# Kernel tuning notes

Hardware: AMD Instinct MI355X
Metric: run time of the kernel (lower is better)

Reference implementation:

```python
import jax, jax.numpy as jnp
import numpy as np


def setup_inputs() -> dict:
    key = jax.random.key(0)
    ks = jax.random.split(key, 6)
    B, N, d = 8, 2048, 64
    h = jax.random.normal(ks[0], (B, N, d), dtype=jnp.float32)
    adj = jax.random.randint(ks[1], (B, N, N), 0, 2, dtype=jnp.int32)
    h_root = jax.random.normal(ks[2], (B, N), dtype=jnp.float32)
    weight = jax.random.normal(ks[3], (d, d), dtype=jnp.float32) * (1.0 / np.sqrt(d))
    a1 = jax.random.normal(ks[4], (d, 1), dtype=jnp.float32) * (1.0 / np.sqrt(d))
    a2 = jax.random.normal(ks[5], (d, 1), dtype=jnp.float32) * (1.0 / np.sqrt(d))
    return {"h": h, "adj": adj, "h_root": h_root, "weight": weight, "a1": a1, "a2": a2}


def reference(h, adj, h_root, weight, a1, a2):
    h0 = h
    hw = jax.nn.relu(jnp.matmul(h, weight))          # (B,N,d)
    t1 = jnp.matmul(hw, a1)                          # (B,N,1)
    t2 = jnp.matmul(hw, a2)                          # (B,N,1)
    # e[b,i,j] = relu(t1[b,i] + t2[b,j])  (broadcast, same as repeat/view in torch)
    e = jax.nn.relu(t1 + jnp.swapaxes(t2, -1, -2))   # (B,N,N)
    # FAITHFUL to source bug: pos0 = -9e15 * zeros_like(adj) == 0, so
    # non-edges get logit 0 (not -inf) before softmax.
    e = jnp.where(adj > 0, e, jnp.zeros_like(e))
    attention = jax.nn.softmax(e, axis=-1)           # (B,N,N)
    embedding = jnp.matmul(attention, hw)            # (B,N,d)
    # assign = h_root[:,:,None] @ ones(B,1,d) -> h_root broadcast over d;
    # assign > 0  <=>  h_root > 0 since ones are positive.
    assign = h_root[:, :, None] * jnp.ones((1, 1, hw.shape[-1]), dtype=hw.dtype)
    embedding = jnp.where(assign > 0, embedding, h0)
    return embedding
```

## Files before the change

### kernel.cpp

```cpp
#include <hip/hip_runtime.h>
#include <hip/hip_bf16.h>

#define BATCH 8
#define NN    2048
#define DD    64
#define BN    (BATCH * NN)

#define NSPLIT 8
#define JSPAN  (NN / NSPLIT)
#define KSTEPS (JSPAN / 32)
#define HWST   264

typedef __attribute__((ext_vector_type(8))) short bf16x8;
typedef __attribute__((ext_vector_type(4))) float f32x4;

static __device__ __forceinline__ unsigned f2bf_pk(float lo, float hi) {
  unsigned ul = __float_as_uint(lo);
  unsigned uh = __float_as_uint(hi);
  ul = (ul + 0x7fffu + ((ul >> 16) & 1u)) >> 16;
  uh = (uh + 0x7fffu + ((uh >> 16) & 1u)) & 0xffff0000u;
  return ul | uh;
}

__global__ __launch_bounds__(256) void k1_hw_t1_t2(
    const float* __restrict__ h, const float* __restrict__ W,
    const float* __restrict__ a1, const float* __restrict__ a2,
    unsigned short* __restrict__ hwT, float* __restrict__ t1, float* __restrict__ t2) {
  __shared__ float ht[64 * 36];
  __shared__ float Ws[64 * 64];
  __shared__ unsigned short bt[64 * 40];

  const int t  = threadIdx.x;
  const int r0 = blockIdx.x * 32;

#pragma unroll
  for (int r = 0; r < 4; ++r) {
    int f = t + 256 * r;
    reinterpret_cast<float4*>(Ws)[f] = reinterpret_cast<const float4*>(W)[f];
  }
#pragma unroll
  for (int r = 0; r < 2; ++r) {
    int f = t + 256 * r;
    int i = f >> 4, j4 = f & 15;
    float4 v = reinterpret_cast<const float4*>(h + (size_t)(r0 + i) * DD)[j4];
    ht[(4 * j4 + 0) * 36 + i] = v.x;
    ht[(4 * j4 + 1) * 36 + i] = v.y;
    ht[(4 * j4 + 2) * 36 + i] = v.z;
    ht[(4 * j4 + 3) * 36 + i] = v.w;
  }
  __syncthreads();

  const int trow = t >> 4, kcol = t & 15;
  float4 acc0 = make_float4(0.f, 0.f, 0.f, 0.f);
  float4 acc1 = make_float4(0.f, 0.f, 0.f, 0.f);

#pragma unroll 8
  for (int j = 0; j < 64; ++j) {
    float2 hv = *reinterpret_cast<const float2*>(&ht[j * 36 + 2 * trow]);
    float4 wv = reinterpret_cast<const float4*>(Ws)[j * 16 + kcol];
    acc0.x = fmaf(hv.x, wv.x, acc0.x); acc0.y = fmaf(hv.x, wv.y, acc0.y);
    acc0.z = fmaf(hv.x, wv.z, acc0.z); acc0.w = fmaf(hv.x, wv.w, acc0.w);
    acc1.x = fmaf(hv.y, wv.x, acc1.x); acc1.y = fmaf(hv.y, wv.y, acc1.y);
    acc1.z = fmaf(hv.y, wv.z, acc1.z); acc1.w = fmaf(hv.y, wv.w, acc1.w);
  }

  acc0.x = fmaxf(acc0.x, 0.f); acc0.y = fmaxf(acc0.y, 0.f);
  acc0.z = fmaxf(acc0.z, 0.f); acc0.w = fmaxf(acc0.w, 0.f);
  acc1.x = fmaxf(acc1.x, 0.f); acc1.y = fmaxf(acc1.y, 0.f);
  acc1.z = fmaxf(acc1.z, 0.f); acc1.w = fmaxf(acc1.w, 0.f);

  float4 a1v = reinterpret_cast<const float4*>(a1)[kcol];
  float4 a2v = reinterpret_cast<const float4*>(a2)[kcol];
  float s1_0 = acc0.x * a1v.x + acc0.y * a1v.y + acc0.z * a1v.z + acc0.w * a1v.w;
  float s1_1 = acc1.x * a1v.x + acc1.y * a1v.y + acc1.z * a1v.z + acc1.w * a1v.w;
  float s2_0 = acc0.x * a2v.x + acc0.y * a2v.y + acc0.z * a2v.z + acc0.w * a2v.w;
  float s2_1 = acc1.x * a2v.x + acc1.y * a2v.y + acc1.z * a2v.z + acc1.w * a2v.w;
#pragma unroll
  for (int m = 1; m <= 8; m <<= 1) {
    s1_0 += __shfl_xor(s1_0, m, 64);
    s1_1 += __shfl_xor(s1_1, m, 64);
    s2_0 += __shfl_xor(s2_0, m, 64);
    s2_1 += __shfl_xor(s2_1, m, 64);
  }
  {
    int row = r0 + 2 * trow;
    if (kcol == 0) {
      t1[row] = s1_0; t1[row + 1] = s1_1;
      t2[row] = s2_0; t2[row + 1] = s2_1;
    }
  }

  {
    const float* a0 = &acc0.x;
    const float* a1p = &acc1.x;
#pragma unroll
    for (int c = 0; c < 4; ++c) {
      int k = 4 * kcol + c;
      *reinterpret_cast<unsigned*>(&bt[k * 40 + 2 * trow]) = f2bf_pk(a0[c], a1p[c]);
    }
  }
  __syncthreads();
  {
    int k = t >> 2, jp = t & 3;
    int bb = r0 >> 11;
    int jb = r0 & (NN - 1);
    *reinterpret_cast<int4*>(hwT + ((size_t)bb * DD + k) * NN + jb + jp * 8) =
        *reinterpret_cast<const int4*>(&bt[k * 40 + jp * 8]);
  }
}

__global__ __launch_bounds__(256, 4) void k2_attn(
    const unsigned short* __restrict__ hwT, const int* __restrict__ adj,
    const float* __restrict__ t1, const float* __restrict__ t2,
    float* __restrict__ pacc, float* __restrict__ pden) {
  __shared__ unsigned short hws[64 * HWST];
  __shared__ float t2s[JSPAN];

  const int t     = threadIdx.x;
  const int split = blockIdx.x >> 8;
  const int rem   = blockIdx.x & 255;
  const int b     = rem >> 5;
  const int i0    = (rem & 31) * 64;
  const int w     = t >> 6;
  const int lane  = t & 63;
  const int m     = lane & 15;
  const int quad  = lane >> 4;
  const int jbase = split * JSPAN;

  const unsigned short* hwTb = hwT + (size_t)b * DD * NN + jbase;
#pragma unroll
  for (int r = 0; r < 8; ++r) {
    int idx = t + 256 * r, k = idx >> 5, jp = idx & 31;
    *reinterpret_cast<int4*>(&hws[k * HWST + jp * 8]) =
        *reinterpret_cast<const int4*>(hwTb + (size_t)k * NN + jp * 8);
  }
  if (t < JSPAN / 4)
    *reinterpret_cast<float4*>(&t2s[t * 4]) =
        *reinterpret_cast<const float4*>(t2 + b * NN + jbase + t * 4);

  const float t1v = t1[b * NN + i0 + w * 16 + m];
  const int* adjl = adj + (size_t)(b * NN + i0 + w * 16 + m) * NN + jbase + quad * 8;

  f32x4 acc[4];
#pragma unroll
  for (int g = 0; g < 4; ++g) acc[g] = (f32x4){0.f, 0.f, 0.f, 0.f};
  float den = 0.f;

  int4 a0 = *reinterpret_cast<const int4*>(adjl);
  int4 a1i = *reinterpret_cast<const int4*>(adjl + 4);
  __syncthreads();

#pragma unroll
  for (int ks = 0; ks < KSTEPS; ++ks) {
    int4 n0, n1;
    if (ks + 1 < KSTEPS) {
      const int* ap = adjl + (ks + 1) * 32;
      n0 = *reinterpret_cast<const int4*>(ap);
      n1 = *reinterpret_cast<const int4*>(ap + 4);
    }

    const float* t2p = &t2s[ks * 32 + quad * 8];
    float4 e0 = *reinterpret_cast<const float4*>(t2p);
    float4 e1 = *reinterpret_cast<const float4*>(t2p + 4);
    float p0 = (a0.x > 0) ? __expf(fmaxf(t1v + e0.x, 0.f)) : 1.f;
    float p1 = (a0.y > 0) ? __expf(fmaxf(t1v + e0.y, 0.f)) : 1.f;
    float p2 = (a0.z > 0) ? __expf(fmaxf(t1v + e0.z, 0.f)) : 1.f;
    float p3 = (a0.w > 0) ? __expf(fmaxf(t1v + e0.w, 0.f)) : 1.f;
    float p4 = (a1i.x > 0) ? __expf(fmaxf(t1v + e1.x, 0.f)) : 1.f;
    float p5 = (a1i.y > 0) ? __expf(fmaxf(t1v + e1.y, 0.f)) : 1.f;
    float p6 = (a1i.z > 0) ? __expf(fmaxf(t1v + e1.z, 0.f)) : 1.f;
    float p7 = (a1i.w > 0) ? __expf(fmaxf(t1v + e1.w, 0.f)) : 1.f;
    den += ((p0 + p1) + (p2 + p3)) + ((p4 + p5) + (p6 + p7));

    union { bf16x8 v; unsigned u[4]; } Af;
    Af.u[0] = f2bf_pk(p0, p1);
    Af.u[1] = f2bf_pk(p2, p3);
    Af.u[2] = f2bf_pk(p4, p5);
    Af.u[3] = f2bf_pk(p6, p7);

#pragma unroll
    for (int g = 0; g < 4; ++g) {
      bf16x8 Bf = *reinterpret_cast<const bf16x8*>(
          &hws[(g * 16 + m) * HWST + ks * 32 + quad * 8]);
      acc[g] = __builtin_amdgcn_mfma_f32_16x16x32_bf16(Af.v, Bf, acc[g], 0, 0, 0);
    }

    a0 = n0; a1i = n1;
  }

  den += __shfl_xor(den, 16, 64);
  den += __shfl_xor(den, 32, 64);

  const size_t sbase = (size_t)split * BN + (size_t)b * NN + i0;
  if (quad == 0) pden[sbase + w * 16 + m] = den;

  __syncthreads();
  float* os = reinterpret_cast<float*>(hws);
#pragma unroll
  for (int g = 0; g < 4; ++g)
#pragma unroll
    for (int r = 0; r < 4; ++r)
      os[(w * 16 + quad * 4 + r) * 68 + g * 16 + m] = acc[g][r];
  __syncthreads();
#pragma unroll
  for (int r2 = 0; r2 < 4; ++r2) {
    int idx = t + 256 * r2, row = idx >> 4, c4 = idx & 15;
    *reinterpret_cast<float4*>(&pacc[(sbase + row) * DD + c4 * 4]) =
        *reinterpret_cast<const float4*>(&os[row * 68 + c4 * 4]);
  }
}

__global__ __launch_bounds__(256) void k3_reduce(
    const float* __restrict__ pacc, const float* __restrict__ pden,
    const float* __restrict__ h, const float* __restrict__ h_root,
    float* __restrict__ out) {
  const int g   = blockIdx.x * 256 + threadIdx.x;
  const int row = g >> 4;
  const int k4  = g & 15;

  float4 a = make_float4(0.f, 0.f, 0.f, 0.f);
  float den = 0.f;
#pragma unroll
  for (int s = 0; s < NSPLIT; ++s) {
    const size_t prow = (size_t)s * BN + row;
    float4 p = reinterpret_cast<const float4*>(pacc + prow * DD)[k4];
    a.x += p.x; a.y += p.y; a.z += p.z; a.w += p.w;
    den += pden[prow];
  }
  const float hr = h_root[row];
  float4 res;
  if (hr > 0.f) {
    const float inv = 1.f / den;
    res.x = a.x * inv; res.y = a.y * inv; res.z = a.z * inv; res.w = a.w * inv;
  } else {
    res = reinterpret_cast<const float4*>(h)[g];
  }
  reinterpret_cast<float4*>(out)[g] = res;
}

extern "C" void kernel_launch(void* const* d_in, const int* in_sizes, int n_in,
                              void* d_out, int out_size, void* d_ws, size_t ws_size,
                              hipStream_t stream) {
  const float* h      = (const float*)d_in[0];
  const int*   adj    = (const int*)d_in[1];
  const float* h_root = (const float*)d_in[2];
  const float* W      = (const float*)d_in[3];
  const float* a1     = (const float*)d_in[4];
  const float* a2     = (const float*)d_in[5];
  float* out = (float*)d_out;

  unsigned short* hwT = (unsigned short*)d_ws;
  float* t1 = (float*)(hwT + (size_t)BN * DD);
  float* t2 = t1 + BN;
  float* pacc = t2 + BN;
  float* pden = pacc + (size_t)NSPLIT * BN * DD;

  k1_hw_t1_t2<<<BN / 32, 256, 0, stream>>>(h, W, a1, a2, hwT, t1, t2);
  k2_attn<<<NSPLIT * 256, 256, 0, stream>>>(hwT, adj, t1, t2, pacc, pden);
  k3_reduce<<<(BN * DD / 4) / 256, 256, 0, stream>>>(pacc, pden, h, h_root, out);
}
```

Measured before the change: 224.4 us.

## Skip adjacency loads for unused rows and process two row tiles per wave

The attention kernel now reads h_root and skips loading adjacency rows whose output will be replaced by the input h. This avoids roughly half of the dominant int32 adjacency traffic. Each wave now handles 32 rows, reusing hw fragments loaded straight from global memory instead of an LDS tile. Partial results are written directly without LDS staging, and the grid is halved. The inner loop is no longer unrolled, and global hw reads may be less coalesced than the previous LDS staging.

```diff
diff --git a/kernel.cpp b/kernel.cpp
--- a/kernel.cpp
+++ b/kernel.cpp
@@ -9,7 +9,6 @@
 #define NSPLIT 8
 #define JSPAN  (NN / NSPLIT)
 #define KSTEPS (JSPAN / 32)
-#define HWST   264
 
 typedef __attribute__((ext_vector_type(8))) short bf16x8;
 typedef __attribute__((ext_vector_type(4))) float f32x4;
@@ -112,102 +111,128 @@
 __global__ __launch_bounds__(256, 4) void k2_attn(
     const unsigned short* __restrict__ hwT, const int* __restrict__ adj,
     const float* __restrict__ t1, const float* __restrict__ t2,
+    const float* __restrict__ h_root,
     float* __restrict__ pacc, float* __restrict__ pden) {
-  __shared__ unsigned short hws[64 * HWST];
   __shared__ float t2s[JSPAN];
 
   const int t     = threadIdx.x;
-  const int split = blockIdx.x >> 8;
-  const int rem   = blockIdx.x & 255;
-  const int b     = rem >> 5;
-  const int i0    = (rem & 31) * 64;
-  const int w     = t >> 6;
+  const int split = blockIdx.x >> 7;
+  const int rem   = blockIdx.x & 127;
+  const int b     = rem >> 4;
+  const int i0    = (rem & 15) * 128 + (t >> 6) * 32;
   const int lane  = t & 63;
   const int m     = lane & 15;
   const int quad  = lane >> 4;
   const int jbase = split * JSPAN;
 
-  const unsigned short* hwTb = hwT + (size_t)b * DD * NN + jbase;
-#pragma unroll
-  for (int r = 0; r < 8; ++r) {
-    int idx = t + 256 * r, k = idx >> 5, jp = idx & 31;
-    *reinterpret_cast<int4*>(&hws[k * HWST + jp * 8]) =
-        *reinterpret_cast<const int4*>(hwTb + (size_t)k * NN + jp * 8);
-  }
   if (t < JSPAN / 4)
     *reinterpret_cast<float4*>(&t2s[t * 4]) =
         *reinterpret_cast<const float4*>(t2 + b * NN + jbase + t * 4);
 
-  const float t1v = t1[b * NN + i0 + w * 16 + m];
-  const int* adjl = adj + (size_t)(b * NN + i0 + w * 16 + m) * NN + jbase + quad * 8;
-
-  f32x4 acc[4];
-#pragma unroll
-  for (int g = 0; g < 4; ++g) acc[g] = (f32x4){0.f, 0.f, 0.f, 0.f};
-  float den = 0.f;
-
-  int4 a0 = *reinterpret_cast<const int4*>(adjl);
-  int4 a1i = *reinterpret_cast<const int4*>(adjl + 4);
+  const int rowbase = b * NN + i0;
+  const float t1v0 = t1[rowbase + m];
+  const float t1v1 = t1[rowbase + 16 + m];
+  const bool  do0  = h_root[rowbase + m] > 0.f;
+  const bool  do1  = h_root[rowbase + 16 + m] > 0.f;
+  const int* adj0 = adj + (size_t)(rowbase + m) * NN + jbase + quad * 8;
+  const int* adj1 = adj + (size_t)(rowbase + 16 + m) * NN + jbase + quad * 8;
+  const unsigned short* hwp = hwT + (size_t)b * DD * NN + jbase + quad * 8 + m * NN;
+
+  f32x4 acc0[4], acc1[4];
+#pragma unroll
+  for (int g = 0; g < 4; ++g) {
+    acc0[g] = (f32x4){0.f, 0.f, 0.f, 0.f};
+    acc1[g] = (f32x4){0.f, 0.f, 0.f, 0.f};
+  }
+  float den0 = 0.f, den1 = 0.f;
+
+  int4 c00 = make_int4(0, 0, 0, 0), c01 = c00, c10 = c00, c11 = c00;
+  if (do0) { c00 = *reinterpret_cast<const int4*>(adj0);
+             c01 = *reinterpret_cast<const int4*>(adj0 + 4); }
+  if (do1) { c10 = *reinterpret_cast<const int4*>(adj1);
+             c11 = *reinterpret_cast<const int4*>(adj1 + 4); }
+
   __syncthreads();
 
-#pragma unroll
+#pragma unroll 1
   for (int ks = 0; ks < KSTEPS; ++ks) {
-    int4 n0, n1;
+    int4 n00 = make_int4(0, 0, 0, 0), n01 = n00, n10 = n00, n11 = n00;
     if (ks + 1 < KSTEPS) {
-      const int* ap = adjl + (ks + 1) * 32;
-      n0 = *reinterpret_cast<const int4*>(ap);
-      n1 = *reinterpret_cast<const int4*>(ap + 4);
-    }
+      const int* a0p = adj0 + (ks + 1) * 32;
+      const int* a1p = adj1 + (ks + 1) * 32;
+      if (do0) { n00 = *reinterpret_cast<const int4*>(a0p);
+                 n01 = *reinterpret_cast<const int4*>(a0p + 4); }
+      if (do1) { n10 = *reinterpret_cast<const int4*>(a1p);
+                 n11 = *reinterpret_cast<const int4*>(a1p + 4); }
+    }
+
+    bf16x8 B0 = *reinterpret_cast<const bf16x8*>(hwp + 0 * 16 * NN + ks * 32);
+    bf16x8 B1 = *reinterpret_cast<const bf16x8*>(hwp + 1 * 16 * NN + ks * 32);
+    bf16x8 B2 = *reinterpret_cast<const bf16x8*>(hwp + 2 * 16 * NN + ks * 32);
+    bf16x8 B3 = *reinterpret_cast<const bf16x8*>(hwp + 3 * 16 * NN + ks * 32);
 
     const float* t2p = &t2s[ks * 32 + quad * 8];
     float4 e0 = *reinterpret_cast<const float4*>(t2p);
     float4 e1 = *reinterpret_cast<const float4*>(t2p + 4);
-    float p0 = (a0.x > 0) ? __expf(fmaxf(t1v + e0.x, 0.f)) : 1.f;
-    float p1 = (a0.y > 0) ? __expf(fmaxf(t1v + e0.y, 0.f)) : 1.f;
-    float p2 = (a0.z > 0) ? __expf(fmaxf(t1v + e0.z, 0.f)) : 1.f;
-    float p3 = (a0.w > 0) ? __expf(fmaxf(t1v + e0.w, 0.f)) : 1.f;
-    float p4 = (a1i.x > 0) ? __expf(fmaxf(t1v + e1.x, 0.f)) : 1.f;
-    float p5 = (a1i.y > 0) ? __expf(fmaxf(t1v + e1.y, 0.f)) : 1.f;
-    float p6 = (a1i.z > 0) ? __expf(fmaxf(t1v + e1.z, 0.f)) : 1.f;
-    float p7 = (a1i.w > 0) ? __expf(fmaxf(t1v + e1.w, 0.f)) : 1.f;
-    den += ((p0 + p1) + (p2 + p3)) + ((p4 + p5) + (p6 + p7));
-
-    union { bf16x8 v; unsigned u[4]; } Af;
-    Af.u[0] = f2bf_pk(p0, p1);
-    Af.u[1] = f2bf_pk(p2, p3);
-    Af.u[2] = f2bf_pk(p4, p5);
-    Af.u[3] = f2bf_pk(p6, p7);
-
-#pragma unroll
-    for (int g = 0; g < 4; ++g) {
-      bf16x8 Bf = *reinterpret_cast<const bf16x8*>(
-          &hws[(g * 16 + m) * HWST + ks * 32 + quad * 8]);
-      acc[g] = __builtin_amdgcn_mfma_f32_16x16x32_bf16(Af.v, Bf, acc[g], 0, 0, 0);
-    }
-
-    a0 = n0; a1i = n1;
-  }
-
-  den += __shfl_xor(den, 16, 64);
-  den += __shfl_xor(den, 32, 64);
-
-  const size_t sbase = (size_t)split * BN + (size_t)b * NN + i0;
-  if (quad == 0) pden[sbase + w * 16 + m] = den;
-
-  __syncthreads();
-  float* os = reinterpret_cast<float*>(hws);
+
+    union { bf16x8 v; unsigned u[4]; } Af0, Af1;
+    {
+      float p0 = (c00.x > 0) ? __expf(fmaxf(t1v0 + e0.x, 0.f)) : 1.f;
+      float p1 = (c00.y > 0) ? __expf(fmaxf(t1v0 + e0.y, 0.f)) : 1.f;
+      float p2 = (c00.z > 0) ? __expf(fmaxf(t1v0 + e0.z, 0.f)) : 1.f;
+      float p3 = (c00.w > 0) ? __expf(fmaxf(t1v0 + e0.w, 0.f)) : 1.f;
+      float p4 = (c01.x > 0) ? __expf(fmaxf(t1v0 + e1.x, 0.f)) : 1.f;
+      float p5 = (c01.y > 0) ? __expf(fmaxf(t1v0 + e1.y, 0.f)) : 1.f;
+      float p6 = (c01.z > 0) ? __expf(fmaxf(t1v0 + e1.z, 0.f)) : 1.f;
+      float p7 = (c01.w > 0) ? __expf(fmaxf(t1v0 + e1.w, 0.f)) : 1.f;
+      den0 += ((p0 + p1) + (p2 + p3)) + ((p4 + p5) + (p6 + p7));
+      Af0.u[0] = f2bf_pk(p0, p1); Af0.u[1] = f2bf_pk(p2, p3);
+      Af0.u[2] = f2bf_pk(p4, p5); Af0.u[3] = f2bf_pk(p6, p7);
+    }
+    {
+      float p0 = (c10.x > 0) ? __expf(fmaxf(t1v1 + e0.x, 0.f)) : 1.f;
+      float p1 = (c10.y > 0) ? __expf(fmaxf(t1v1 + e0.y, 0.f)) : 1.f;
+      float p2 = (c10.z > 0) ? __expf(fmaxf(t1v1 + e0.z, 0.f)) : 1.f;
+      float p3 = (c10.w > 0) ? __expf(fmaxf(t1v1 + e0.w, 0.f)) : 1.f;
+      float p4 = (c11.x > 0) ? __expf(fmaxf(t1v1 + e1.x, 0.f)) : 1.f;
+      float p5 = (c11.y > 0) ? __expf(fmaxf(t1v1 + e1.y, 0.f)) : 1.f;
+      float p6 = (c11.z > 0) ? __expf(fmaxf(t1v1 + e1.z, 0.f)) : 1.f;
+      float p7 = (c11.w > 0) ? __expf(fmaxf(t1v1 + e1.w, 0.f)) : 1.f;
+      den1 += ((p0 + p1) + (p2 + p3)) + ((p4 + p5) + (p6 + p7));
+      Af1.u[0] = f2bf_pk(p0, p1); Af1.u[1] = f2bf_pk(p2, p3);
+      Af1.u[2] = f2bf_pk(p4, p5); Af1.u[3] = f2bf_pk(p6, p7);
+    }
+
+    acc0[0] = __builtin_amdgcn_mfma_f32_16x16x32_bf16(Af0.v, B0, acc0[0], 0, 0, 0);
+    acc0[1] = __builtin_amdgcn_mfma_f32_16x16x32_bf16(Af0.v, B1, acc0[1], 0, 0, 0);
+    acc0[2] = __builtin_amdgcn_mfma_f32_16x16x32_bf16(Af0.v, B2, acc0[2], 0, 0, 0);
+    acc0[3] = __builtin_amdgcn_mfma_f32_16x16x32_bf16(Af0.v, B3, acc0[3], 0, 0, 0);
+    acc1[0] = __builtin_amdgcn_mfma_f32_16x16x32_bf16(Af1.v, B0, acc1[0], 0, 0, 0);
+    acc1[1] = __builtin_amdgcn_mfma_f32_16x16x32_bf16(Af1.v, B1, acc1[1], 0, 0, 0);
+    acc1[2] = __builtin_amdgcn_mfma_f32_16x16x32_bf16(Af1.v, B2, acc1[2], 0, 0, 0);
+    acc1[3] = __builtin_amdgcn_mfma_f32_16x16x32_bf16(Af1.v, B3, acc1[3], 0, 0, 0);
+
+    c00 = n00; c01 = n01; c10 = n10; c11 = n11;
+  }
+
+  den0 += __shfl_xor(den0, 16, 64);
+  den0 += __shfl_xor(den0, 32, 64);
+  den1 += __shfl_xor(den1, 16, 64);
+  den1 += __shfl_xor(den1, 32, 64);
+
+  const size_t sbase = (size_t)split * BN + rowbase;
+  if (quad == 0) {
+    pden[sbase + m] = den0;
+    pden[sbase + 16 + m] = den1;
+  }
+
 #pragma unroll
   for (int g = 0; g < 4; ++g)
 #pragma unroll
-    for (int r = 0; r < 4; ++r)
-      os[(w * 16 + quad * 4 + r) * 68 + g * 16 + m] = acc[g][r];
-  __syncthreads();
-#pragma unroll
-  for (int r2 = 0; r2 < 4; ++r2) {
-    int idx = t + 256 * r2, row = idx >> 4, c4 = idx & 15;
-    *reinterpret_cast<float4*>(&pacc[(sbase + row) * DD + c4 * 4]) =
-        *reinterpret_cast<const float4*>(&os[row * 68 + c4 * 4]);
-  }
+    for (int r = 0; r < 4; ++r) {
+      pacc[(sbase + quad * 4 + r) * DD + g * 16 + m] = acc0[g][r];
+      pacc[(sbase + 16 + quad * 4 + r) * DD + g * 16 + m] = acc1[g][r];
+    }
 }
 
 __global__ __launch_bounds__(256) void k3_reduce(
@@ -256,6 +281,6 @@
   float* pden = pacc + (size_t)NSPLIT * BN * DD;
 
   k1_hw_t1_t2<<<BN / 32, 256, 0, stream>>>(h, W, a1, a2, hwT, t1, t2);
-  k2_attn<<<NSPLIT * 256, 256, 0, stream>>>(hwT, adj, t1, t2, pacc, pden);
+  k2_attn<<<NSPLIT * 128, 256, 0, stream>>>(hwT, adj, t1, t2, h_root, pacc, pden);
   k3_reduce<<<(BN * DD / 4) / 256, 256, 0, stream>>>(pacc, pden, h, h_root, out);
 }
```

Result: faster. 217.4 us (-3.1%).

## Fuse split-K reduction into attention kernel and skip adjacency loads for inactive rows

Applied to the files above, without the earlier changes.

The attention kernel now gives each block 16 rows and splits the column range across its four waves. The waves' partial accumulators and denominators are combined in shared memory, and the output is written directly, so the separate reduce kernel and the large partial-sum buffers are gone. Adjacency loads are skipped for rows whose h_root is not positive, since those outputs take h unchanged. The register prefetch depth grows to two steps. hw tiles are now read straight from global memory instead of being staged in shared memory, which risks more cache traffic and less latency hiding.

```diff
diff --git a/kernel.cpp b/kernel.cpp
--- a/kernel.cpp
+++ b/kernel.cpp
@@ -6,10 +6,8 @@
 #define DD    64
 #define BN    (BATCH * NN)
 
-#define NSPLIT 8
-#define JSPAN  (NN / NSPLIT)
+#define JSPAN  (NN / 4)
 #define KSTEPS (JSPAN / 32)
-#define HWST   264
 
 typedef __attribute__((ext_vector_type(8))) short bf16x8;
 typedef __attribute__((ext_vector_type(4))) float f32x4;
@@ -112,130 +110,118 @@
 __global__ __launch_bounds__(256, 4) void k2_attn(
     const unsigned short* __restrict__ hwT, const int* __restrict__ adj,
     const float* __restrict__ t1, const float* __restrict__ t2,
-    float* __restrict__ pacc, float* __restrict__ pden) {
-  __shared__ unsigned short hws[64 * HWST];
-  __shared__ float t2s[JSPAN];
-
-  const int t     = threadIdx.x;
-  const int split = blockIdx.x >> 8;
-  const int rem   = blockIdx.x & 255;
-  const int b     = rem >> 5;
-  const int i0    = (rem & 31) * 64;
-  const int w     = t >> 6;
-  const int lane  = t & 63;
-  const int m     = lane & 15;
-  const int quad  = lane >> 4;
-  const int jbase = split * JSPAN;
-
-  const unsigned short* hwTb = hwT + (size_t)b * DD * NN + jbase;
-#pragma unroll
-  for (int r = 0; r < 8; ++r) {
-    int idx = t + 256 * r, k = idx >> 5, jp = idx & 31;
-    *reinterpret_cast<int4*>(&hws[k * HWST + jp * 8]) =
-        *reinterpret_cast<const int4*>(hwTb + (size_t)k * NN + jp * 8);
-  }
-  if (t < JSPAN / 4)
-    *reinterpret_cast<float4*>(&t2s[t * 4]) =
-        *reinterpret_cast<const float4*>(t2 + b * NN + jbase + t * 4);
-
-  const float t1v = t1[b * NN + i0 + w * 16 + m];
-  const int* adjl = adj + (size_t)(b * NN + i0 + w * 16 + m) * NN + jbase + quad * 8;
+    const float* __restrict__ h, const float* __restrict__ h_root,
+    float* __restrict__ out) {
+  __shared__ float t2s[NN];
+  __shared__ float os[4][16][68];
+  __shared__ float denos[4][16];
+
+  const int t    = threadIdx.x;
+  const int b    = blockIdx.x >> 7;
+  const int i0   = (blockIdx.x & 127) * 16;
+  const int w    = t >> 6;
+  const int lane = t & 63;
+  const int m    = lane & 15;
+  const int quad = lane >> 4;
+  const int jbase = w * JSPAN;
+
+#pragma unroll
+  for (int r = 0; r < 2; ++r)
+    reinterpret_cast<float4*>(t2s)[t + 256 * r] =
+        reinterpret_cast<const float4*>(t2 + b * NN)[t + 256 * r];
+
+  const int rowbase = b * NN + i0;
+  const float t1v = t1[rowbase + m];
+  const bool  act = h_root[rowbase + m] > 0.f;
+  const int* adjl = adj + (size_t)(rowbase + m) * NN + jbase + quad * 8;
+  const unsigned short* hwp = hwT + (size_t)b * DD * NN + jbase + quad * 8 + m * NN;
 
   f32x4 acc[4];
 #pragma unroll
   for (int g = 0; g < 4; ++g) acc[g] = (f32x4){0.f, 0.f, 0.f, 0.f};
   float den = 0.f;
 
-  int4 a0 = *reinterpret_cast<const int4*>(adjl);
-  int4 a1i = *reinterpret_cast<const int4*>(adjl + 4);
-  __syncthreads();
-
-#pragma unroll
+  int4 c0 = make_int4(0,0,0,0), c1 = c0, n10 = c0, n11 = c0, n20, n21;
+  if (act) {
+    c0  = *reinterpret_cast<const int4*>(adjl);
+    c1  = *reinterpret_cast<const int4*>(adjl + 4);
+    n10 = *reinterpret_cast<const int4*>(adjl + 32);
+    n11 = *reinterpret_cast<const int4*>(adjl + 36);
+  }
+
+  __syncthreads();
+
+#pragma unroll 1
   for (int ks = 0; ks < KSTEPS; ++ks) {
-    int4 n0, n1;
-    if (ks + 1 < KSTEPS) {
-      const int* ap = adjl + (ks + 1) * 32;
-      n0 = *reinterpret_cast<const int4*>(ap);
-      n1 = *reinterpret_cast<const int4*>(ap + 4);
-    }
-
-    const float* t2p = &t2s[ks * 32 + quad * 8];
+    n20 = make_int4(0,0,0,0); n21 = n20;
+    if (ks + 2 < KSTEPS && act) {
+      const int* ap = adjl + (ks + 2) * 32;
+      n20 = *reinterpret_cast<const int4*>(ap);
+      n21 = *reinterpret_cast<const int4*>(ap + 4);
+    }
+
+    bf16x8 B0 = *reinterpret_cast<const bf16x8*>(hwp + 0 * 16 * NN + ks * 32);
+    bf16x8 B1 = *reinterpret_cast<const bf16x8*>(hwp + 1 * 16 * NN + ks * 32);
+    bf16x8 B2 = *reinterpret_cast<const bf16x8*>(hwp + 2 * 16 * NN + ks * 32);
+    bf16x8 B3 = *reinterpret_cast<const bf16x8*>(hwp + 3 * 16 * NN + ks * 32);
+
+    const float* t2p = &t2s[jbase + ks * 32 + quad * 8];
     float4 e0 = *reinterpret_cast<const float4*>(t2p);
     float4 e1 = *reinterpret_cast<const float4*>(t2p + 4);
-    float p0 = (a0.x > 0) ? __expf(fmaxf(t1v + e0.x, 0.f)) : 1.f;
-    float p1 = (a0.y > 0) ? __expf(fmaxf(t1v + e0.y, 0.f)) : 1.f;
-    float p2 = (a0.z > 0) ? __expf(fmaxf(t1v + e0.z, 0.f)) : 1.f;
-    float p3 = (a0.w > 0) ? __expf(fmaxf(t1v + e0.w, 0.f)) : 1.f;
-    float p4 = (a1i.x > 0) ? __expf(fmaxf(t1v + e1.x, 0.f)) : 1.f;
-    float p5 = (a1i.y > 0) ? __expf(fmaxf(t1v + e1.y, 0.f)) : 1.f;
-    float p6 = (a1i.z > 0) ? __expf(fmaxf(t1v + e1.z, 0.f)) : 1.f;
-    float p7 = (a1i.w > 0) ? __expf(fmaxf(t1v + e1.w, 0.f)) : 1.f;
+
+    float p0 = (c0.x > 0) ? __expf(fmaxf(t1v + e0.x, 0.f)) : 1.f;
+    float p1 = (c0.y > 0) ? __expf(fmaxf(t1v + e0.y, 0.f)) : 1.f;
+    float p2 = (c0.z > 0) ? __expf(fmaxf(t1v + e0.z, 0.f)) : 1.f;
+    float p3 = (c0.w > 0) ? __expf(fmaxf(t1v + e0.w, 0.f)) : 1.f;
+    float p4 = (c1.x > 0) ? __expf(fmaxf(t1v + e1.x, 0.f)) : 1.f;
+    float p5 = (c1.y > 0) ? __expf(fmaxf(t1v + e1.y, 0.f)) : 1.f;
+    float p6 = (c1.z > 0) ? __expf(fmaxf(t1v + e1.z, 0.f)) : 1.f;
+    float p7 = (c1.w > 0) ? __expf(fmaxf(t1v + e1.w, 0.f)) : 1.f;
     den += ((p0 + p1) + (p2 + p3)) + ((p4 + p5) + (p6 + p7));
 
     union { bf16x8 v; unsigned u[4]; } Af;
-    Af.u[0] = f2bf_pk(p0, p1);
-    Af.u[1] = f2bf_pk(p2, p3);
-    Af.u[2] = f2bf_pk(p4, p5);
-    Af.u[3] = f2bf_pk(p6, p7);
-
-#pragma unroll
-    for (int g = 0; g < 4; ++g) {
-      bf16x8 Bf = *reinterpret_cast<const bf16x8*>(
-          &hws[(g * 16 + m) * HWST + ks * 32 + quad * 8]);
-      acc[g] = __builtin_amdgcn_mfma_f32_16x16x32_bf16(Af.v, Bf, acc[g], 0, 0, 0);
-    }
-
-    a0 = n0; a1i = n1;
+    Af.u[0] = f2bf_pk(p0, p1); Af.u[1] = f2bf_pk(p2, p3);
+    Af.u[2] = f2bf_pk(p4, p5); Af.u[3] = f2bf_pk(p6, p7);
+
+    acc[0] = __builtin_amdgcn_mfma_f32_16x16x32_bf16(Af.v, B0, acc[0], 0, 0, 0);
+    acc[1] = __builtin_amdgcn_mfma_f32_16x16x32_bf16(Af.v, B1, acc[1], 0, 0, 0);
+    acc[2] = __builtin_amdgcn_mfma_f32_16x16x32_bf16(Af.v, B2, acc[2], 0, 0, 0);
+    acc[3] = __builtin_amdgcn_mfma_f32_16x16x32_bf16(Af.v, B3, acc[3], 0, 0, 0);
+
+    c0 = n10; c1 = n11; n10 = n20; n11 = n21;
   }
 
   den += __shfl_xor(den, 16, 64);
   den += __shfl_xor(den, 32, 64);
-
-  const size_t sbase = (size_t)split * BN + (size_t)b * NN + i0;
-  if (quad == 0) pden[sbase + w * 16 + m] = den;
-
-  __syncthreads();
-  float* os = reinterpret_cast<float*>(hws);
+  if (quad == 0) denos[w][m] = den;
+
 #pragma unroll
   for (int g = 0; g < 4; ++g)
 #pragma unroll
     for (int r = 0; r < 4; ++r)
-      os[(w * 16 + quad * 4 + r) * 68 + g * 16 + m] = acc[g][r];
-  __syncthreads();
-#pragma unroll
-  for (int r2 = 0; r2 < 4; ++r2) {
-    int idx = t + 256 * r2, row = idx >> 4, c4 = idx & 15;
-    *reinterpret_cast<float4*>(&pacc[(sbase + row) * DD + c4 * 4]) =
-        *reinterpret_cast<const float4*>(&os[row * 68 + c4 * 4]);
-  }
-}
-
-__global__ __launch_bounds__(256) void k3_reduce(
-    const float* __restrict__ pacc, const float* __restrict__ pden,
-    const float* __restrict__ h, const float* __restrict__ h_root,
-    float* __restrict__ out) {
-  const int g   = blockIdx.x * 256 + threadIdx.x;
-  const int row = g >> 4;
-  const int k4  = g & 15;
-
-  float4 a = make_float4(0.f, 0.f, 0.f, 0.f);
-  float den = 0.f;
-#pragma unroll
-  for (int s = 0; s < NSPLIT; ++s) {
-    const size_t prow = (size_t)s * BN + row;
-    float4 p = reinterpret_cast<const float4*>(pacc + prow * DD)[k4];
-    a.x += p.x; a.y += p.y; a.z += p.z; a.w += p.w;
-    den += pden[prow];
-  }
-  const float hr = h_root[row];
-  float4 res;
-  if (hr > 0.f) {
-    const float inv = 1.f / den;
-    res.x = a.x * inv; res.y = a.y * inv; res.z = a.z * inv; res.w = a.w * inv;
-  } else {
-    res = reinterpret_cast<const float4*>(h)[g];
-  }
-  reinterpret_cast<float4*>(out)[g] = res;
+      os[w][quad * 4 + r][g * 16 + m] = acc[g][r];
+  __syncthreads();
+
+  {
+    const int i = t >> 4, k4 = t & 15;
+    float4 a = make_float4(0.f, 0.f, 0.f, 0.f);
+    float d = 0.f;
+#pragma unroll
+    for (int ww = 0; ww < 4; ++ww) {
+      float4 p = *reinterpret_cast<const float4*>(&os[ww][i][k4 * 4]);
+      a.x += p.x; a.y += p.y; a.z += p.z; a.w += p.w;
+      d += denos[ww][i];
+    }
+    const size_t row = (size_t)rowbase + i;
+    float4 res;
+    if (h_root[row] > 0.f) {
+      const float inv = 1.f / d;
+      res.x = a.x * inv; res.y = a.y * inv; res.z = a.z * inv; res.w = a.w * inv;
+    } else {
+      res = reinterpret_cast<const float4*>(h + row * DD)[k4];
+    }
+    reinterpret_cast<float4*>(out + row * DD)[k4] = res;
+  }
 }
 
 extern "C" void kernel_launch(void* const* d_in, const int* in_sizes, int n_in,
@@ -252,10 +238,7 @@
   unsigned short* hwT = (unsigned short*)d_ws;
   float* t1 = (float*)(hwT + (size_t)BN * DD);
   float* t2 = t1 + BN;
-  float* pacc = t2 + BN;
-  float* pden = pacc + (size_t)NSPLIT * BN * DD;
 
   k1_hw_t1_t2<<<BN / 32, 256, 0, stream>>>(h, W, a1, a2, hwT, t1, t2);
-  k2_attn<<<NSPLIT * 256, 256, 0, stream>>>(hwT, adj, t1, t2, pacc, pden);
-  k3_reduce<<<(BN * DD / 4) / 256, 256, 0, stream>>>(pacc, pden, h, h_root, out);
-}
+  k2_attn<<<BATCH * (NN / 16), 256, 0, stream>>>(hwT, adj, t1, t2, h, h_root, out);
+}
```

Measured after the change: 225.0 us. No clear change (+0.3%).
